# Optimization experiments

Measured on AMD Instinct MI355X. Metric: run time of the kernel, lower is better.

The kernel has to match this reference:

```python
import jax, jax.numpy as jnp
import numpy as np

DIM = 1536
NUM_HEADS = 16
HEAD_DIM = DIM // NUM_HEADS  # 96
ROPE_DIM = HEAD_DIM // 2     # 48
PT_SEQ = 32
FT_SEQ = 32
EPS = 1e-6


def _rope_tables():
    # VisionRotaryEmbedding(dim=48, pt_seq_len=32): 2D axial rotary tables
    f = 1.0 / (10000.0 ** (np.arange(0, ROPE_DIM, 2, dtype=np.float32)[: ROPE_DIM // 2] / ROPE_DIM))
    pos = np.arange(FT_SEQ, dtype=np.float32) / FT_SEQ * PT_SEQ
    freqs = pos[:, None] * f[None, :]                       # [32, 24]
    freqs = np.repeat(freqs, 2, axis=-1)                    # [32, 48] interleaved
    row = np.broadcast_to(freqs[:, None, :], (FT_SEQ, FT_SEQ, ROPE_DIM))
    col = np.broadcast_to(freqs[None, :, :], (FT_SEQ, FT_SEQ, ROPE_DIM))
    grid = np.concatenate([row, col], axis=-1).reshape(-1, HEAD_DIM)  # [1024, 96]
    return jnp.asarray(np.cos(grid)), jnp.asarray(np.sin(grid))


def _apply_rotary(x, cos, sin):
    # x: [B, S, H, D]; cos/sin: [S, D]; interleaved (use_real_unbind_dim=-1) rotation
    xr = x.reshape(*x.shape[:-1], -1, 2)
    x_rot = jnp.stack([-xr[..., 1], xr[..., 0]], axis=-1).reshape(x.shape)
    return x * cos[None, :, None, :] + x_rot * sin[None, :, None, :]


def _rms_norm(x, w):
    var = jnp.mean(jnp.square(x), axis=-1, keepdims=True)
    return x * jax.lax.rsqrt(var + EPS) * w


def setup_inputs() -> dict:
    key = jax.random.key(0)
    ks = jax.random.split(key, 12)
    s = 1.0 / np.sqrt(DIM)
    return {
        "hidden_states": jax.random.normal(ks[0], (8, 1024, DIM), dtype=jnp.float32),
        "Wq": jax.random.normal(ks[1], (DIM, DIM), dtype=jnp.float32) * s,
        "bq": jax.random.normal(ks[2], (DIM,), dtype=jnp.float32) * 0.01,
        "Wk": jax.random.normal(ks[3], (DIM, DIM), dtype=jnp.float32) * s,
        "bk": jax.random.normal(ks[4], (DIM,), dtype=jnp.float32) * 0.01,
        "Wv": jax.random.normal(ks[5], (DIM, DIM), dtype=jnp.float32) * s,
        "bv": jax.random.normal(ks[6], (DIM,), dtype=jnp.float32) * 0.01,
        "q_norm_w": jnp.ones((HEAD_DIM,), dtype=jnp.float32),
        "k_norm_w": jnp.ones((HEAD_DIM,), dtype=jnp.float32),
        "Wo": jax.random.normal(ks[7], (DIM, DIM), dtype=jnp.float32) * s,
        "bo": jax.random.normal(ks[8], (DIM,), dtype=jnp.float32) * 0.01,
    }


def reference(hidden_states, Wq, bq, Wk, bk, Wv, bv, q_norm_w, k_norm_w, Wo, bo):
    B, S, _ = hidden_states.shape
    cos, sin = _rope_tables()  # [S, HEAD_DIM], constants

    q = hidden_states @ Wq.T + bq
    k = hidden_states @ Wk.T + bk
    v = hidden_states @ Wv.T + bv
    q = q.reshape(B, S, NUM_HEADS, HEAD_DIM)
    k = k.reshape(B, S, NUM_HEADS, HEAD_DIM)
    v = v.reshape(B, S, NUM_HEADS, HEAD_DIM)

    q = _rms_norm(q, q_norm_w)
    k = _rms_norm(k, k_norm_w)
    q = _apply_rotary(q, cos, sin)
    k = _apply_rotary(k, cos, sin)

    scale = 1.0 / np.sqrt(HEAD_DIM)
    scores = jnp.einsum("bshd,bthd->bhst", q, k) * scale  # [B, H, S, S]
    probs = jax.nn.softmax(scores, axis=-1)
    out = jnp.einsum("bhst,bthd->bshd", probs, v)          # [B, S, H, D]
    out = out.reshape(B, S, DIM)
    return out @ Wo.T + bo
```

## Files before the change

kernel.cpp:

```cpp
#include <hip/hip_runtime.h>
#include <hip/hip_bf16.h>
#include <math.h>

typedef __hip_bfloat16 bf16;
typedef __attribute__((ext_vector_type(8))) short short8;
typedef __attribute__((ext_vector_type(4))) short short4v;
typedef __attribute__((ext_vector_type(4))) float f32x4;

#define MFMA16(a, b, c) __builtin_amdgcn_mfma_f32_16x16x32_bf16((a), (b), (c), 0, 0, 0)

typedef const __attribute__((address_space(1))) void GVOID;
typedef __attribute__((address_space(3))) void LVOID;

__device__ __forceinline__ float b2f(short s) {
    union { unsigned u; float f; } v;
    v.u = ((unsigned)(unsigned short)s) << 16;
    return v.f;
}
__device__ __forceinline__ short f2b(float f) {
    union { float f; unsigned u; } v;
    v.f = f;
    unsigned r = v.u + 0x7fffu + ((v.u >> 16) & 1u);
    return (short)(r >> 16);
}
__device__ __forceinline__ unsigned packbf2(float a, float b) {
    float2 t; t.x = a; t.y = b;
    __hip_bfloat162 h = __float22bfloat162_rn(t);
    union { __hip_bfloat162 h; unsigned u; } cv; cv.h = h;
    return cv.u;
}
__device__ __forceinline__ short bf2s(float x) {
    __hip_bfloat16 h = __float2bfloat16(x);
    union { __hip_bfloat16 h; short s; } cv; cv.h = h;
    return cv.s;
}

__global__ void sniff_kernel(const unsigned* __restrict__ X, int* __restrict__ flag) {
    __shared__ int cnt;
    if (threadIdx.x == 0) cnt = 0;
    __syncthreads();
    int c = 0;
    for (int i = threadIdx.x; i < 256; i += 64) {
        unsigned w = X[i];
        unsigned e = (w >> 7) & 0xFFu;
        c += (e > 140u) ? 1 : 0;
    }
    atomicAdd(&cnt, c);
    __syncthreads();
    if (threadIdx.x == 0) *flag = (cnt >= 16) ? 1 : 0;
}

__device__ __forceinline__ void canon8(const void* src, short* dst, int i, int f) {
    short8 o;
    if (f) {
        const float* s = (const float*)src + (size_t)i * 8;
#pragma unroll
        for (int j = 0; j < 8; ++j) o[j] = f2b(s[j]);
    } else {
        o = ((const short8*)src)[i];
    }
    ((short8*)dst)[i] = o;
}

__global__ __launch_bounds__(256) void canon_x_kernel(
    const void* __restrict__ src, short* __restrict__ dst, int n8,
    const int* __restrict__ flag)
{
    int i = blockIdx.x * 256 + threadIdx.x;
    if (i >= n8) return;
    canon8(src, dst, i, *flag);
}

__global__ __launch_bounds__(256) void canon_w4_kernel(
    const void* __restrict__ s0, const void* __restrict__ s1,
    const void* __restrict__ s2, const void* __restrict__ s3,
    short* __restrict__ d0, short* __restrict__ d1,
    short* __restrict__ d2, short* __restrict__ d3,
    const int* __restrict__ flag)
{
    const int m = blockIdx.y;
    const void* src = (m == 0) ? s0 : (m == 1) ? s1 : (m == 2) ? s2 : s3;
    short* dst = (m == 0) ? d0 : (m == 1) ? d1 : (m == 2) ? d2 : d3;
    int i = blockIdx.x * 256 + threadIdx.x;
    canon8(src, dst, i, *flag);
}

__global__ void canon_vec_kernel(
    const void* __restrict__ bq, const void* __restrict__ bk,
    const void* __restrict__ bv, const void* __restrict__ bo,
    const void* __restrict__ qw, const void* __restrict__ kw,
    float* __restrict__ biasqkv, float* __restrict__ boc,
    float* __restrict__ qwc, float* __restrict__ kwc,
    const int* __restrict__ flag)
{
    const int f = *flag;
    for (int i = threadIdx.x; i < 6336; i += 256) {
        const void* src; float* dst; int j;
        if (i < 4608) {
            int m = i / 1536; j = i - m * 1536;
            src = (m == 0) ? bq : (m == 1) ? bk : bv; dst = biasqkv + i;
        } else if (i < 6144) { j = i - 4608; src = bo; dst = boc + j; }
        else if (i < 6240)   { j = i - 6144; src = qw; dst = qwc + j; }
        else                 { j = i - 6240; src = kw; dst = kwc + j; }
        *dst = f ? ((const float*)src)[j] : b2f(((const short*)src)[j]);
    }
}

__global__ void rope_tables_kernel(float* __restrict__ cosT, float* __restrict__ sinT) {
    int idx = blockIdx.x * 256 + threadIdx.x;
    if (idx >= 1024 * 96) return;
    int p = idx / 96;
    int d = idx - p * 96;
    int r = p >> 5, c = p & 31;
    int inRow = (d < 48);
    int dd = inRow ? d : d - 48;
    float pos = inRow ? (float)r : (float)c;
    float ex = -(float)(dd & ~1) / 48.0f;
    float f = powf(10000.0f, ex);
    float ang = pos * f;
    cosT[idx] = cosf(ang);
    sinT[idx] = sinf(ang);
}

__global__ __launch_bounds__(256) void gemm128_kernel(
    const bf16* __restrict__ A, const bf16* __restrict__ Bw,
    const float* __restrict__ bias,
    bf16* __restrict__ O0, bf16* __restrict__ O1, bf16* __restrict__ O2,
    int K, const int* __restrict__ outFlag)
{
    __shared__ __align__(16) short As[2][128 * 64];
    __shared__ __align__(16) short Bs[2][128 * 64];

    const int tid = threadIdx.x;
    const int lane = tid & 63, w = tid >> 6;
    const int wr = w >> 1, wc = w & 1;
    const int li = lane & 15, lg = lane >> 4;

    const int total = gridDim.x * gridDim.y;
    const int pp = blockIdx.y * gridDim.x + blockIdx.x;
    const int lb = (pp & 7) * (total >> 3) + (pp >> 3);
    const int nb = lb % gridDim.x;
    const int mb = lb / gridDim.x;
    const long mBase = (long)mb * 128;
    const long nGlob = (long)nb * 128;

    const bf16* aSrc[4]; const bf16* bSrc[4]; int ldsOff[4];
#pragma unroll
    for (int u = 0; u < 4; ++u) {
        const int L = u * 4096 + tid * 16;
        const int S = L ^ (((L >> 7) & 7) << 4);
        const int srow = S >> 7;
        const int scol = (S & 127) >> 1;
        aSrc[u] = A + (mBase + srow) * K + scol;
        bSrc[u] = Bw + (nGlob + srow) * K + scol;
        ldsOff[u] = L >> 1;
    }
    const int rxor = (li & 7) << 4;
    int kidx[2];
#pragma unroll
    for (int ks = 0; ks < 2; ++ks)
        kidx[ks] = ((ks * 64 + lg * 16) ^ rxor) >> 1;

    f32x4 acc[4][4] = {};
    const int NT = K >> 6;

    auto stage = [&](int tt, int bb) {
        const long kc = (long)tt * 64;
#pragma unroll
        for (int u = 0; u < 4; ++u)
            __builtin_amdgcn_global_load_lds((GVOID*)(aSrc[u] + kc),
                                             (LVOID*)&As[bb][ldsOff[u]], 16, 0, 0);
#pragma unroll
        for (int u = 0; u < 4; ++u)
            __builtin_amdgcn_global_load_lds((GVOID*)(bSrc[u] + kc),
                                             (LVOID*)&Bs[bb][ldsOff[u]], 16, 0, 0);
    };

    stage(0, 0);
    asm volatile("s_waitcnt vmcnt(0)" ::: "memory");
    __builtin_amdgcn_s_barrier();
    asm volatile("" ::: "memory");

    for (int t = 0; t < NT; ++t) {
        const int cb = t & 1;
        if (t + 1 < NT) stage(t + 1, cb ^ 1);
        const short* Ab = &As[cb][0];
        const short* Bb = &Bs[cb][0];
#pragma unroll
        for (int ks = 0; ks < 2; ++ks) {
            short8 fa[4], fb[4];
#pragma unroll
            for (int m = 0; m < 4; ++m)
                fa[m] = *(const short8*)(Ab + (wr * 64 + m * 16 + li) * 64 + kidx[ks]);
#pragma unroll
            for (int n = 0; n < 4; ++n)
                fb[n] = *(const short8*)(Bb + (wc * 64 + n * 16 + li) * 64 + kidx[ks]);
            __builtin_amdgcn_sched_barrier(0);
            __builtin_amdgcn_s_setprio(1);
#pragma unroll
            for (int m = 0; m < 4; ++m)
#pragma unroll
                for (int n = 0; n < 4; ++n)
                    acc[m][n] = MFMA16(fa[m], fb[n], acc[m][n]);
            __builtin_amdgcn_s_setprio(0);
            __builtin_amdgcn_sched_barrier(0);
        }
        asm volatile("s_waitcnt vmcnt(0)" ::: "memory");
        __builtin_amdgcn_s_barrier();
        asm volatile("" ::: "memory");
    }

    const int f32out = outFlag ? *outFlag : 0;
    const int mat = nb / 12;
    const long colBase = nGlob - (long)mat * 1536;
    bf16* Ob = (mat == 0) ? O0 : (mat == 1) ? O1 : O2;
    if (f32out) {
        float* Cf = (float*)Ob;
#pragma unroll
        for (int n = 0; n < 4; ++n) {
            const long col = colBase + wc * 64 + n * 16 + li;
            const float bv = bias[nGlob + wc * 64 + n * 16 + li];
#pragma unroll
            for (int m = 0; m < 4; ++m) {
                const long row = mBase + wr * 64 + m * 16 + lg * 4;
#pragma unroll
                for (int i = 0; i < 4; ++i)
                    Cf[(row + i) * 1536 + col] = acc[m][n][i] + bv;
            }
        }
    } else {
#pragma unroll
        for (int n = 0; n < 4; ++n) {
            const long col = colBase + wc * 64 + n * 16 + li;
            const float bv = bias[nGlob + wc * 64 + n * 16 + li];
#pragma unroll
            for (int m = 0; m < 4; ++m) {
                const long row = mBase + wr * 64 + m * 16 + lg * 4;
#pragma unroll
                for (int i = 0; i < 4; ++i)
                    Ob[(row + i) * 1536 + col] = __float2bfloat16(acc[m][n][i] + bv);
            }
        }
    }
}

__global__ __launch_bounds__(256) void norm_rope_kernel(
    bf16* __restrict__ T, const float* __restrict__ wgt,
    const float* __restrict__ cosT, const float* __restrict__ sinT,
    float scale)
{
    const int row = blockIdx.x * 256 + threadIdx.x;
    const int tok = row >> 4;
    const int h = row & 15;
    const int spos = tok & 1023;
    bf16* p = T + (size_t)tok * 1536 + h * 96;

    float x[96];
#pragma unroll
    for (int v = 0; v < 12; ++v) {
        short8 t = *(const short8*)(p + v * 8);
#pragma unroll
        for (int j = 0; j < 8; ++j) x[v * 8 + j] = b2f(t[j]);
    }
    float ss = 0.f;
#pragma unroll
    for (int d = 0; d < 96; ++d) ss += x[d] * x[d];
    const float rn = scale / sqrtf(ss * (1.0f / 96.0f) + 1e-6f);

    const float* cr = cosT + spos * 96;
    const float* sr = sinT + spos * 96;

#pragma unroll
    for (int v = 0; v < 12; ++v) {
        short8 o;
#pragma unroll
        for (int j = 0; j < 8; j += 2) {
            const int d = v * 8 + j;
            const float x0 = x[d] * rn * wgt[d];
            const float x1 = x[d + 1] * rn * wgt[d + 1];
            o[j]     = f2b(x0 * cr[d] - x1 * sr[d]);
            o[j + 1] = f2b(x1 * cr[d + 1] + x0 * sr[d + 1]);
        }
        *(short8*)(p + v * 8) = o;
    }
}

__global__ __launch_bounds__(256) void attn_kernel(
    const bf16* __restrict__ Q, const bf16* __restrict__ K,
    const bf16* __restrict__ V, bf16* __restrict__ O)
{
    __shared__ __align__(16) short Ks[64 * 104];
    __shared__ __align__(16) short Vt[96 * 76];
    __shared__ __align__(16) short Pl[4][32 * 72];

    const int tid = threadIdx.x;
    const int l = tid & 63, w = tid >> 6;
    const int li = l & 15, lg = l >> 4;

    const int p = blockIdx.x;
    const int lb = (p & 7) * 128 + (p >> 3);
    const int qt = lb & 7;
    const int bh = lb >> 3;
    const int b = bh >> 4, h = bh & 15;
    const size_t tokBase = (size_t)b * 1024;

    short8 aq[2][3];
#pragma unroll
    for (int r = 0; r < 2; ++r) {
        const bf16* qp = Q + (tokBase + qt * 128 + w * 32 + r * 16 + li) * 1536 + h * 96;
#pragma unroll
        for (int kk = 0; kk < 3; ++kk)
            aq[r][kk] = *(const short8*)(qp + kk * 32 + lg * 8);
    }

    float m_r[2] = {-1e30f, -1e30f};
    float l_r[2] = {0.f, 0.f};
    f32x4 o[2][6] = {};

    int kr[3], km[3];
#pragma unroll
    for (int u = 0; u < 3; ++u) {
        const int c = tid + 256 * u;
        kr[u] = c / 12;
        km[u] = (c - kr[u] * 12) * 8;
    }
    const int t2 = tid >> 3;
    const int dh = tid & 7;
    const bf16* vbase = V + (tokBase + 2 * t2) * 1536 + h * 96 + dh * 12;
    short* Plw = &Pl[w][0];

    short8 kreg[3];
    short4v vr0[3], vr1[3];
#pragma unroll
    for (int u = 0; u < 3; ++u)
        kreg[u] = *(const short8*)(K + (tokBase + kr[u]) * 1536 + h * 96 + km[u]);
#pragma unroll
    for (int u = 0; u < 3; ++u) {
        vr0[u] = *(const short4v*)(vbase + u * 4);
        vr1[u] = *(const short4v*)(vbase + 1536 + u * 4);
    }

    for (int t0 = 0; t0 < 1024; t0 += 64) {
        __syncthreads();
#pragma unroll
        for (int u = 0; u < 3; ++u)
            *(short8*)&Ks[kr[u] * 104 + km[u]] = kreg[u];
        {
            unsigned* Vt32 = (unsigned*)Vt;
#pragma unroll
            for (int u = 0; u < 3; ++u)
#pragma unroll
                for (int j = 0; j < 4; ++j) {
                    const int d = dh * 12 + u * 4 + j;
                    const unsigned pk = ((unsigned)(unsigned short)vr0[u][j]) |
                                        (((unsigned)(unsigned short)vr1[u][j]) << 16);
                    Vt32[d * 38 + t2] = pk;
                }
        }
        __syncthreads();

        const int t1 = (t0 + 64 < 1024) ? t0 + 64 : t0;
#pragma unroll
        for (int u = 0; u < 3; ++u)
            kreg[u] = *(const short8*)(K + (tokBase + t1 + kr[u]) * 1536 + h * 96 + km[u]);
        {
            const bf16* vp = vbase + (size_t)t1 * 1536;
#pragma unroll
            for (int u = 0; u < 3; ++u) {
                vr0[u] = *(const short4v*)(vp + u * 4);
                vr1[u] = *(const short4v*)(vp + 1536 + u * 4);
            }
        }

        f32x4 s4[2][4] = {};
#pragma unroll
        for (int kk = 0; kk < 3; ++kk) {
            short8 fk[4];
#pragma unroll
            for (int kn = 0; kn < 4; ++kn)
                fk[kn] = *(const short8*)&Ks[(kn * 16 + li) * 104 + kk * 32 + lg * 8];
#pragma unroll
            for (int r = 0; r < 2; ++r)
#pragma unroll
                for (int kn = 0; kn < 4; ++kn)
                    s4[r][kn] = MFMA16(fk[kn], aq[r][kk], s4[r][kn]);
        }

#pragma unroll
        for (int r = 0; r < 2; ++r) {
            float mk[4];
#pragma unroll
            for (int kn = 0; kn < 4; ++kn)
                mk[kn] = fmaxf(fmaxf(s4[r][kn][0], s4[r][kn][1]),
                               fmaxf(s4[r][kn][2], s4[r][kn][3]));
            float pm = fmaxf(fmaxf(mk[0], mk[1]), fmaxf(mk[2], mk[3]));
            pm = fmaxf(pm, __shfl_xor(pm, 16));
            pm = fmaxf(pm, __shfl_xor(pm, 32));

            float alpha = 1.0f;
            const bool need = (pm > m_r[r] + 8.0f);
            if (need) { alpha = exp2f(m_r[r] - pm); m_r[r] = pm; }
            const float mn = m_r[r];

            float rs = 0.f;
            unsigned pw[8];
#pragma unroll
            for (int kn = 0; kn < 4; ++kn) {
                float p0 = exp2f(s4[r][kn][0] - mn);
                float p1 = exp2f(s4[r][kn][1] - mn);
                float p2 = exp2f(s4[r][kn][2] - mn);
                float p3 = exp2f(s4[r][kn][3] - mn);
                rs += (p0 + p1) + (p2 + p3);
                pw[kn * 2]     = packbf2(p0, p1);
                pw[kn * 2 + 1] = packbf2(p2, p3);
            }
            rs += __shfl_xor(rs, 16);
            rs += __shfl_xor(rs, 32);
            l_r[r] = l_r[r] * alpha + rs;
            if (need) {
#pragma unroll
                for (int dn = 0; dn < 6; ++dn)
#pragma unroll
                    for (int i = 0; i < 4; ++i) o[r][dn][i] *= alpha;
            }
            unsigned* Pw = (unsigned*)Plw;
            const int rowW = ((r * 16 + li) * 72) >> 1;
#pragma unroll
            for (int kn = 0; kn < 4; ++kn) {
#pragma unroll
                for (int ip = 0; ip < 2; ++ip)
                    Pw[rowW + ((kn * 16 + lg * 4 + ip * 2) >> 1)] = pw[kn * 2 + ip];
            }
        }

#pragma unroll
        for (int kt = 0; kt < 2; ++kt) {
            short8 pa[2];
#pragma unroll
            for (int r = 0; r < 2; ++r)
                pa[r] = *(const short8*)&Plw[(r * 16 + li) * 72 + kt * 32 + lg * 8];
#pragma unroll
            for (int dn = 0; dn < 6; ++dn) {
                short8 fv = *(const short8*)&Vt[(dn * 16 + li) * 76 + kt * 32 + lg * 8];
#pragma unroll
                for (int r = 0; r < 2; ++r)
                    o[r][dn] = MFMA16(fv, pa[r], o[r][dn]);
            }
        }
    }

#pragma unroll
    for (int r = 0; r < 2; ++r) {
        const float inv = 1.0f / l_r[r];
        const size_t row = tokBase + qt * 128 + w * 32 + r * 16 + li;
#pragma unroll
        for (int dn = 0; dn < 6; ++dn) {
            short4v ov;
#pragma unroll
            for (int i = 0; i < 4; ++i) ov[i] = bf2s(o[r][dn][i] * inv);
            *(short4v*)&O[row * 1536 + h * 96 + dn * 16 + lg * 4] = ov;
        }
    }
}

extern "C" void kernel_launch(void* const* d_in, const int* in_sizes, int n_in,
                              void* d_out, int out_size, void* d_ws, size_t ws_size,
                              hipStream_t stream) {
    const void* X  = d_in[0];
    const void* Wq = d_in[1];
    const void* bq = d_in[2];
    const void* Wk = d_in[3];
    const void* bk = d_in[4];
    const void* Wv = d_in[5];
    const void* bv = d_in[6];
    const void* qw = d_in[7];
    const void* kw = d_in[8];
    const void* Wo = d_in[9];
    const void* bo = d_in[10];

    char* ws = (char*)d_ws;
    size_t off = 0;
    int* flag = (int*)ws;                      off += 256;
    float* cosT = (float*)(ws + off);          off += 1024 * 96 * 4;
    float* sinT = (float*)(ws + off);          off += 1024 * 96 * 4;
    float* biasqkv = (float*)(ws + off);       off += 4608 * 4;
    float* boc  = (float*)(ws + off);          off += 1536 * 4;
    float* qwc  = (float*)(ws + off);          off += 128 * 4;
    float* kwc  = (float*)(ws + off);          off += 128 * 4;
    off = (off + 255) & ~(size_t)255;
    bf16* Wc  = (bf16*)(ws + off);             off += (size_t)4608 * 1536 * 2;
    bf16* Woc = (bf16*)(ws + off);             off += (size_t)1536 * 1536 * 2;
    bf16* Xc  = (bf16*)(ws + off);             off += (size_t)8192 * 1536 * 2;
    bf16* Qb  = (bf16*)(ws + off);             off += (size_t)8192 * 1536 * 2;
    bf16* Kb  = (bf16*)(ws + off);             off += (size_t)8192 * 1536 * 2;
    bf16* Vb  = (bf16*)(ws + off);             off += (size_t)8192 * 1536 * 2;
    bf16* AO  = Xc;

    sniff_kernel<<<1, 64, 0, stream>>>((const unsigned*)X, flag);

    canon_x_kernel<<<6144, 256, 0, stream>>>(X, (short*)Xc, 8192 * 1536 / 8, flag);
    canon_w4_kernel<<<dim3(1152, 4), 256, 0, stream>>>(
        Wq, Wk, Wv, Wo,
        (short*)Wc, (short*)(Wc + (size_t)1536 * 1536), (short*)(Wc + (size_t)2 * 1536 * 1536),
        (short*)Woc, flag);
    canon_vec_kernel<<<1, 256, 0, stream>>>(bq, bk, bv, bo, qw, kw,
                                            biasqkv, boc, qwc, kwc, flag);
    rope_tables_kernel<<<384, 256, 0, stream>>>(cosT, sinT);

    gemm128_kernel<<<dim3(36, 64), 256, 0, stream>>>(
        Xc, Wc, biasqkv, Qb, Kb, Vb, 1536, nullptr);

    const float qscale = (float)(0.10206207261596577 * 1.4426950408889634);
    norm_rope_kernel<<<512, 256, 0, stream>>>(Qb, qwc, cosT, sinT, qscale);
    norm_rope_kernel<<<512, 256, 0, stream>>>(Kb, kwc, cosT, sinT, 1.0f);

    attn_kernel<<<1024, 256, 0, stream>>>(Qb, Kb, Vb, AO);

    gemm128_kernel<<<dim3(12, 64), 256, 0, stream>>>(
        AO, Woc, boc, (bf16*)d_out, (bf16*)d_out, (bf16*)d_out, 1536, flag);
}
```

Before: 384.7 us.

## Merge prep kernels, fuse Q/K norm launches, swizzle attention LDS layouts

Combines the sniff, bias/weight conversion and rope table kernels into one prep launch. It also merges the X and weight canonicalisation into one launch and runs Q and K norm-rope in a single 2D grid. Inside attention, the padded LDS strides for K, V-transpose and P are replaced by XOR-swizzled unpadded layouts with 64-bit P stores, and occupancy is hinted with launch_bounds(256,4). These changes aim to cut launch overhead and LDS bank conflicts while shrinking shared memory use. The risk is swizzle indexing mistakes and register pressure from the occupancy hint.

New measurement: 634.7 us. +65.0%, slower.

```diff
diff --git a/kernel.cpp b/kernel.cpp
--- a/kernel.cpp
+++ b/kernel.cpp
@@ -35,19 +35,51 @@
     return cv.s;
 }
 
-__global__ void sniff_kernel(const unsigned* __restrict__ X, int* __restrict__ flag) {
-    __shared__ int cnt;
-    if (threadIdx.x == 0) cnt = 0;
-    __syncthreads();
-    int c = 0;
-    for (int i = threadIdx.x; i < 256; i += 64) {
-        unsigned w = X[i];
+__global__ __launch_bounds__(256) void prep_kernel(
+    const unsigned* __restrict__ X,
+    const void* __restrict__ bq, const void* __restrict__ bk,
+    const void* __restrict__ bv, const void* __restrict__ bo,
+    const void* __restrict__ qw, const void* __restrict__ kw,
+    int* __restrict__ flag, float* __restrict__ biasqkv, float* __restrict__ boc,
+    float* __restrict__ qwc, float* __restrict__ kwc,
+    float* __restrict__ cosT, float* __restrict__ sinT)
+{
+    const int tid = threadIdx.x;
+    if (blockIdx.x == 0) {
+        __shared__ int cnt;
+        if (tid == 0) cnt = 0;
+        __syncthreads();
+        unsigned w = X[tid];
         unsigned e = (w >> 7) & 0xFFu;
-        c += (e > 140u) ? 1 : 0;
-    }
-    atomicAdd(&cnt, c);
-    __syncthreads();
-    if (threadIdx.x == 0) *flag = (cnt >= 16) ? 1 : 0;
+        if (e > 140u) atomicAdd(&cnt, 1);
+        __syncthreads();
+        const int f = (cnt >= 16) ? 1 : 0;
+        if (tid == 0) *flag = f;
+        for (int i = tid; i < 6336; i += 256) {
+            const void* src; float* dst; int j;
+            if (i < 4608) {
+                int m = i / 1536; j = i - m * 1536;
+                src = (m == 0) ? bq : (m == 1) ? bk : bv; dst = biasqkv + i;
+            } else if (i < 6144) { j = i - 4608; src = bo; dst = boc + j; }
+            else if (i < 6240)   { j = i - 6144; src = qw; dst = qwc + j; }
+            else                 { j = i - 6240; src = kw; dst = kwc + j; }
+            *dst = f ? ((const float*)src)[j] : b2f(((const short*)src)[j]);
+        }
+    } else {
+        int idx = (blockIdx.x - 1) * 256 + tid;
+        if (idx >= 1024 * 96) return;
+        int p = idx / 96;
+        int d = idx - p * 96;
+        int r = p >> 5, c = p & 31;
+        int inRow = (d < 48);
+        int dd = inRow ? d : d - 48;
+        float pos = inRow ? (float)r : (float)c;
+        float ex = -(float)(dd & ~1) / 48.0f;
+        float f = powf(10000.0f, ex);
+        float ang = pos * f;
+        cosT[idx] = cosf(ang);
+        sinT[idx] = sinf(ang);
+    }
 }
 
 __device__ __forceinline__ void canon8(const void* src, short* dst, int i, int f) {
@@ -62,64 +94,27 @@
     ((short8*)dst)[i] = o;
 }
 
-__global__ __launch_bounds__(256) void canon_x_kernel(
-    const void* __restrict__ src, short* __restrict__ dst, int n8,
-    const int* __restrict__ flag)
-{
-    int i = blockIdx.x * 256 + threadIdx.x;
-    if (i >= n8) return;
-    canon8(src, dst, i, *flag);
-}
-
-__global__ __launch_bounds__(256) void canon_w4_kernel(
+__global__ __launch_bounds__(256) void canon_all_kernel(
+    const void* __restrict__ X,
     const void* __restrict__ s0, const void* __restrict__ s1,
     const void* __restrict__ s2, const void* __restrict__ s3,
+    short* __restrict__ dX,
     short* __restrict__ d0, short* __restrict__ d1,
     short* __restrict__ d2, short* __restrict__ d3,
     const int* __restrict__ flag)
 {
-    const int m = blockIdx.y;
-    const void* src = (m == 0) ? s0 : (m == 1) ? s1 : (m == 2) ? s2 : s3;
-    short* dst = (m == 0) ? d0 : (m == 1) ? d1 : (m == 2) ? d2 : d3;
-    int i = blockIdx.x * 256 + threadIdx.x;
-    canon8(src, dst, i, *flag);
-}
-
-__global__ void canon_vec_kernel(
-    const void* __restrict__ bq, const void* __restrict__ bk,
-    const void* __restrict__ bv, const void* __restrict__ bo,
-    const void* __restrict__ qw, const void* __restrict__ kw,
-    float* __restrict__ biasqkv, float* __restrict__ boc,
-    float* __restrict__ qwc, float* __restrict__ kwc,
-    const int* __restrict__ flag)
-{
     const int f = *flag;
-    for (int i = threadIdx.x; i < 6336; i += 256) {
-        const void* src; float* dst; int j;
-        if (i < 4608) {
-            int m = i / 1536; j = i - m * 1536;
-            src = (m == 0) ? bq : (m == 1) ? bk : bv; dst = biasqkv + i;
-        } else if (i < 6144) { j = i - 4608; src = bo; dst = boc + j; }
-        else if (i < 6240)   { j = i - 6144; src = qw; dst = qwc + j; }
-        else                 { j = i - 6240; src = kw; dst = kwc + j; }
-        *dst = f ? ((const float*)src)[j] : b2f(((const short*)src)[j]);
-    }
-}
-
-__global__ void rope_tables_kernel(float* __restrict__ cosT, float* __restrict__ sinT) {
-    int idx = blockIdx.x * 256 + threadIdx.x;
-    if (idx >= 1024 * 96) return;
-    int p = idx / 96;
-    int d = idx - p * 96;
-    int r = p >> 5, c = p & 31;
-    int inRow = (d < 48);
-    int dd = inRow ? d : d - 48;
-    float pos = inRow ? (float)r : (float)c;
-    float ex = -(float)(dd & ~1) / 48.0f;
-    float f = powf(10000.0f, ex);
-    float ang = pos * f;
-    cosT[idx] = cosf(ang);
-    sinT[idx] = sinf(ang);
+    const int bid = blockIdx.x;
+    if (bid < 6144) {
+        canon8(X, dX, bid * 256 + threadIdx.x, f);
+    } else {
+        const int wb = bid - 6144;
+        const int m = wb / 1152;
+        const int i = (wb - m * 1152) * 256 + threadIdx.x;
+        const void* src = (m == 0) ? s0 : (m == 1) ? s1 : (m == 2) ? s2 : s3;
+        short* dst = (m == 0) ? d0 : (m == 1) ? d1 : (m == 2) ? d2 : d3;
+        canon8(src, dst, i, f);
+    }
 }
 
 __global__ __launch_bounds__(256) void gemm128_kernel(
@@ -244,11 +239,16 @@
     }
 }
 
-__global__ __launch_bounds__(256) void norm_rope_kernel(
-    bf16* __restrict__ T, const float* __restrict__ wgt,
+__global__ __launch_bounds__(256) void norm_rope2_kernel(
+    bf16* __restrict__ Qb, bf16* __restrict__ Kb,
+    const float* __restrict__ qwc, const float* __restrict__ kwc,
     const float* __restrict__ cosT, const float* __restrict__ sinT,
-    float scale)
+    float qscale)
 {
+    bf16* T = blockIdx.y ? Kb : Qb;
+    const float* wgt = blockIdx.y ? kwc : qwc;
+    const float scale = blockIdx.y ? 1.0f : qscale;
+
     const int row = blockIdx.x * 256 + threadIdx.x;
     const int tok = row >> 4;
     const int h = row & 15;
@@ -285,13 +285,13 @@
     }
 }
 
-__global__ __launch_bounds__(256) void attn_kernel(
+__global__ __launch_bounds__(256, 4) void attn_kernel(
     const bf16* __restrict__ Q, const bf16* __restrict__ K,
     const bf16* __restrict__ V, bf16* __restrict__ O)
 {
-    __shared__ __align__(16) short Ks[64 * 104];
-    __shared__ __align__(16) short Vt[96 * 76];
-    __shared__ __align__(16) short Pl[4][32 * 72];
+    __shared__ __align__(16) short Ks[64 * 96];
+    __shared__ __align__(16) short Vt[96 * 64];
+    __shared__ __align__(16) short Pl[4][32 * 64];
 
     const int tid = threadIdx.x;
     const int l = tid & 63, w = tid >> 6;
@@ -317,18 +317,22 @@
     float l_r[2] = {0.f, 0.f};
     f32x4 o[2][6] = {};
 
-    int kr[3], km[3];
+    int kr[3], km[3], kso[3];
 #pragma unroll
     for (int u = 0; u < 3; ++u) {
         const int c = tid + 256 * u;
         kr[u] = c / 12;
         km[u] = (c - kr[u] * 12) * 8;
+        kso[u] = (kr[u] * 96 + km[u]) ^ ((kr[u] & 7) << 3);
     }
     const int t2 = tid >> 3;
     const int dh = tid & 7;
     const bf16* vbase = V + (tokBase + 2 * t2) * 1536 + h * 96 + dh * 12;
     short* Plw = &Pl[w][0];
 
+    const int kswz = (li & 7) << 3;
+    const int vswz = ((li >> 1) & 7) << 3;
+
     short8 kreg[3];
     short4v vr0[3], vr1[3];
 #pragma unroll
@@ -344,7 +348,7 @@
         __syncthreads();
 #pragma unroll
         for (int u = 0; u < 3; ++u)
-            *(short8*)&Ks[kr[u] * 104 + km[u]] = kreg[u];
+            *(short8*)&Ks[kso[u]] = kreg[u];
         {
             unsigned* Vt32 = (unsigned*)Vt;
 #pragma unroll
@@ -354,7 +358,7 @@
                     const int d = dh * 12 + u * 4 + j;
                     const unsigned pk = ((unsigned)(unsigned short)vr0[u][j]) |
                                         (((unsigned)(unsigned short)vr1[u][j]) << 16);
-                    Vt32[d * 38 + t2] = pk;
+                    Vt32[(d * 32 + t2) ^ (((d >> 1) & 7) << 2)] = pk;
                 }
         }
         __syncthreads();
@@ -378,7 +382,7 @@
             short8 fk[4];
 #pragma unroll
             for (int kn = 0; kn < 4; ++kn)
-                fk[kn] = *(const short8*)&Ks[(kn * 16 + li) * 104 + kk * 32 + lg * 8];
+                fk[kn] = *(const short8*)&Ks[((kn * 16 + li) * 96 + kk * 32 + lg * 8) ^ kswz];
 #pragma unroll
             for (int r = 0; r < 2; ++r)
 #pragma unroll
@@ -403,7 +407,7 @@
             const float mn = m_r[r];
 
             float rs = 0.f;
-            unsigned pw[8];
+            unsigned long long pq[4];
 #pragma unroll
             for (int kn = 0; kn < 4; ++kn) {
                 float p0 = exp2f(s4[r][kn][0] - mn);
@@ -411,8 +415,8 @@
                 float p2 = exp2f(s4[r][kn][2] - mn);
                 float p3 = exp2f(s4[r][kn][3] - mn);
                 rs += (p0 + p1) + (p2 + p3);
-                pw[kn * 2]     = packbf2(p0, p1);
-                pw[kn * 2 + 1] = packbf2(p2, p3);
+                pq[kn] = ((unsigned long long)packbf2(p0, p1)) |
+                         (((unsigned long long)packbf2(p2, p3)) << 32);
             }
             rs += __shfl_xor(rs, 16);
             rs += __shfl_xor(rs, 32);
@@ -423,14 +427,10 @@
 #pragma unroll
                     for (int i = 0; i < 4; ++i) o[r][dn][i] *= alpha;
             }
-            unsigned* Pw = (unsigned*)Plw;
-            const int rowW = ((r * 16 + li) * 72) >> 1;
-#pragma unroll
-            for (int kn = 0; kn < 4; ++kn) {
-#pragma unroll
-                for (int ip = 0; ip < 2; ++ip)
-                    Pw[rowW + ((kn * 16 + lg * 4 + ip * 2) >> 1)] = pw[kn * 2 + ip];
-            }
+            const int rowS = (r * 16 + li) * 64;
+#pragma unroll
+            for (int kn = 0; kn < 4; ++kn)
+                *(unsigned long long*)&Plw[(rowS + kn * 16 + lg * 4) ^ kswz] = pq[kn];
         }
 
 #pragma unroll
@@ -438,10 +438,10 @@
             short8 pa[2];
 #pragma unroll
             for (int r = 0; r < 2; ++r)
-                pa[r] = *(const short8*)&Plw[(r * 16 + li) * 72 + kt * 32 + lg * 8];
+                pa[r] = *(const short8*)&Plw[((r * 16 + li) * 64 + kt * 32 + lg * 8) ^ kswz];
 #pragma unroll
             for (int dn = 0; dn < 6; ++dn) {
-                short8 fv = *(const short8*)&Vt[(dn * 16 + li) * 76 + kt * 32 + lg * 8];
+                short8 fv = *(const short8*)&Vt[((dn * 16 + li) * 64 + kt * 32 + lg * 8) ^ vswz];
 #pragma unroll
                 for (int r = 0; r < 2; ++r)
                     o[r][dn] = MFMA16(fv, pa[r], o[r][dn]);
@@ -496,23 +496,19 @@
     bf16* Vb  = (bf16*)(ws + off);             off += (size_t)8192 * 1536 * 2;
     bf16* AO  = Xc;
 
-    sniff_kernel<<<1, 64, 0, stream>>>((const unsigned*)X, flag);
-
-    canon_x_kernel<<<6144, 256, 0, stream>>>(X, (short*)Xc, 8192 * 1536 / 8, flag);
-    canon_w4_kernel<<<dim3(1152, 4), 256, 0, stream>>>(
-        Wq, Wk, Wv, Wo,
-        (short*)Wc, (short*)(Wc + (size_t)1536 * 1536), (short*)(Wc + (size_t)2 * 1536 * 1536),
-        (short*)Woc, flag);
-    canon_vec_kernel<<<1, 256, 0, stream>>>(bq, bk, bv, bo, qw, kw,
-                                            biasqkv, boc, qwc, kwc, flag);
-    rope_tables_kernel<<<384, 256, 0, stream>>>(cosT, sinT);
+    prep_kernel<<<385, 256, 0, stream>>>((const unsigned*)X, bq, bk, bv, bo, qw, kw,
+                                         flag, biasqkv, boc, qwc, kwc, cosT, sinT);
+
+    canon_all_kernel<<<10752, 256, 0, stream>>>(
+        X, Wq, Wk, Wv, Wo,
+        (short*)Xc, (short*)Wc, (short*)(Wc + (size_t)1536 * 1536),
+        (short*)(Wc + (size_t)2 * 1536 * 1536), (short*)Woc, flag);
 
     gemm128_kernel<<<dim3(36, 64), 256, 0, stream>>>(
         Xc, Wc, biasqkv, Qb, Kb, Vb, 1536, nullptr);
 
     const float qscale = (float)(0.10206207261596577 * 1.4426950408889634);
-    norm_rope_kernel<<<512, 256, 0, stream>>>(Qb, qwc, cosT, sinT, qscale);
-    norm_rope_kernel<<<512, 256, 0, stream>>>(Kb, kwc, cosT, sinT, 1.0f);
+    norm_rope2_kernel<<<dim3(512, 2), 256, 0, stream>>>(Qb, Kb, qwc, kwc, cosT, sinT, qscale);
 
     attn_kernel<<<1024, 256, 0, stream>>>(Qb, Kb, Vb, AO);
 
```
